# Performance work log

Measured on AMD Instinct MI355X. Metric: run time of the kernel, lower is better.

Reference implementation:

```python
import jax, jax.numpy as jnp
import numpy as np

D_MODEL = 1024
NUM_HEADS = 16
HEAD_DIM = 64
INNER = NUM_HEADS * HEAD_DIM


def setup_inputs() -> dict:
    key = jax.random.key(0)
    k_x, k_q, k_k, k_v, k_o = jax.random.split(key, 5)
    B, T = 4, 2048
    s = 1.0 / np.sqrt(D_MODEL)
    return {
        "x": jax.random.normal(k_x, (B, T, D_MODEL), dtype=jnp.float32),
        "W_q": jax.random.uniform(k_q, (D_MODEL, INNER), dtype=jnp.float32, minval=-s, maxval=s),
        "W_k": jax.random.uniform(k_k, (D_MODEL, INNER), dtype=jnp.float32, minval=-s, maxval=s),
        "W_v": jax.random.uniform(k_v, (D_MODEL, INNER), dtype=jnp.float32, minval=-s, maxval=s),
        "W_o": jax.random.uniform(k_o, (INNER, D_MODEL), dtype=jnp.float32, minval=-s, maxval=s),
    }


def reference(x, W_q, W_k, W_v, W_o):
    B, T, _ = x.shape
    scale = HEAD_DIM ** -0.5
    # project and split heads: [B, H, T, Dh]
    q = (x @ W_q).reshape(B, T, NUM_HEADS, HEAD_DIM).transpose(0, 2, 1, 3)
    k = (x @ W_k).reshape(B, T, NUM_HEADS, HEAD_DIM).transpose(0, 2, 1, 3)
    v = (x @ W_v).reshape(B, T, NUM_HEADS, HEAD_DIM).transpose(0, 2, 1, 3)
    scores = jnp.einsum("bhqd,bhkd->bhqk", q, k) * scale  # [B,H,T,T]
    causal = jnp.tril(jnp.ones((T, T), dtype=bool))
    scores = jnp.where(causal, scores, -jnp.inf)
    probs = jax.nn.softmax(scores, axis=-1)
    ctx = jnp.einsum("bhqk,bhkd->bhqd", probs, v)
    ctx = ctx.transpose(0, 2, 1, 3).reshape(B, T, INNER)
    return ctx @ W_o
```

## Files before the change

kernel.cpp:

```cpp
#include <hip/hip_runtime.h>


typedef short  short8  __attribute__((ext_vector_type(8)));
typedef short  short4v __attribute__((ext_vector_type(4)));
typedef float  floatx4 __attribute__((ext_vector_type(4)));
typedef unsigned uint2v __attribute__((ext_vector_type(2)));
typedef unsigned uintx4 __attribute__((ext_vector_type(4)));

#define T_SZ 2048
#define DM   1024

#define QSCALE 0.18033688011112042f

__device__ __forceinline__ short f2bf(float f) {
  unsigned u = __float_as_uint(f);
  u += 0x7fffu + ((u >> 16) & 1u);
  return (short)(u >> 16);
}

#if defined(__has_builtin) && __has_builtin(__builtin_amdgcn_cvt_pk_bf16_f32)
typedef __bf16 bf16x2_t __attribute__((ext_vector_type(2)));
__device__ __forceinline__ unsigned pack_bf(float lo, float hi) {
  return __builtin_bit_cast(unsigned, __builtin_amdgcn_cvt_pk_bf16_f32(lo, hi));
}
#else
__device__ __forceinline__ unsigned pack_bf(float lo, float hi) {
  return __builtin_amdgcn_perm(__float_as_uint(hi) + 0x8000u,
                               __float_as_uint(lo) + 0x8000u, 0x07060302u);
}
#endif

#if defined(__has_builtin) && __has_builtin(__builtin_amdgcn_exp2f)
__device__ __forceinline__ float fexp2(float x) { return __builtin_amdgcn_exp2f(x); }
#else
__device__ __forceinline__ float fexp2(float x) { return exp2f(x); }
#endif

#if defined(__has_builtin)
#if __has_builtin(__builtin_amdgcn_permlane32_swap) && __has_builtin(__builtin_amdgcn_permlane16_swap)
#define HAVE_PLSWAP 1
#endif
#endif

#ifdef HAVE_PLSWAP
__device__ __forceinline__ short8 pswap_build(unsigned w0, unsigned w1,
                                              unsigned w2, unsigned w3) {
  auto r02 = __builtin_amdgcn_permlane32_swap(w0, w2, false, false);
  auto r13 = __builtin_amdgcn_permlane32_swap(w1, w3, false, false);
  auto d02 = __builtin_amdgcn_permlane16_swap(r02[0], r02[1], false, false);
  auto d13 = __builtin_amdgcn_permlane16_swap(r13[0], r13[1], false, false);
  uintx4 pd;
  pd.x = d02[0]; pd.y = d13[0]; pd.z = d02[1]; pd.w = d13[1];
  return __builtin_bit_cast(short8, pd);
}
#endif

__device__ __forceinline__ void gll16(const void* g, void* l) {
  __builtin_amdgcn_global_load_lds((const __attribute__((address_space(1))) void*)g,
                                   (__attribute__((address_space(3))) void*)l, 16, 0, 0);
}

#define SBAR() asm volatile("s_barrier" ::: "memory")
#define WLG()  asm volatile("s_waitcnt lgkmcnt(0)" ::: "memory")
#define WV6()  asm volatile("s_waitcnt vmcnt(6)" ::: "memory")
#define WV0()  asm volatile("s_waitcnt vmcnt(0)" ::: "memory")

__global__ void cvt_kernel(const float* __restrict__ s0, const float* __restrict__ s1,
                           const float* __restrict__ s2, const float* __restrict__ s3,
                           short* __restrict__ dst,
                           const float* __restrict__ x, short* __restrict__ xb) {
  const int tx = threadIdx.x, ty = threadIdx.y;
  if (blockIdx.z == 4) {
    const int tid = ty * 32 + tx;
    const int blk = blockIdx.y * 32 + blockIdx.x;
    int i = (blk * 256 + tid) * 4;
#pragma unroll
    for (int j = 0; j < 8; ++j) {
      const float4 v = *(const float4*)(x + i);
      short4v o;
      o.x = f2bf(v.x); o.y = f2bf(v.y); o.z = f2bf(v.z); o.w = f2bf(v.w);
      *(short4v*)(xb + i) = o;
      i += 1048576;
    }
    return;
  }
  const float* srcs[4] = {s0, s1, s2, s3};
  const float* src = srcs[blockIdx.z];
  short* d = dst + (size_t)blockIdx.z * 1048576;
  __shared__ float tile[32][33];
  const int n_base = blockIdx.x * 32, k_base = blockIdx.y * 32;
#pragma unroll
  for (int j = 0; j < 4; ++j)
    tile[ty + j * 8][tx] = src[(size_t)(k_base + ty + j * 8) * 1024 + n_base + tx];
  __syncthreads();
#pragma unroll
  for (int j = 0; j < 4; ++j)
    d[(size_t)(n_base + ty + j * 8) * 1024 + k_base + tx] = f2bf(tile[tx][ty + j * 8]);
}

__global__ __launch_bounds__(512, 2) void gemm_qkvT(
    const short* __restrict__ Wt, const short* __restrict__ xb,
    short* __restrict__ obf, short* __restrict__ vt) {
  __shared__ short As[2 * 128 * 64];
  __shared__ short Bs[2 * 256 * 64];
  const int tid  = threadIdx.x;
  const int w    = tid >> 6, lane = tid & 63;
  const int quad = lane >> 4, l15 = lane & 15;
  const int wr   = w >> 2, wc = w & 3;
  const int fx   = l15 & 7;
  const int lid  = (int)blockIdx.x;
  const int xcd  = lid & 7, idx = lid >> 3;
  const int m0   = (idx >> 2) * 128;
  const int n0   = (xcd * 4 + (idx & 3)) * 256;
  const int srow = tid >> 3;
  const int scol = ((tid & 7) ^ (srow & 7)) * 8;

  const short* Ag = Wt + (size_t)(m0 + srow) * 1024 + scol;
  const short* Bg = xb + (size_t)(n0 + srow) * 1024 + scol;

  floatx4 acc[4][4] = {};
  short8 af[2][2], bf[4][2];

#define STG_A(slot, kb) do { \
    short* _lb = &As[(slot) * 8192 + tid * 8]; \
    gll16(Ag + (kb), _lb); \
    gll16(Ag + (size_t)(64 * 1024) + (kb), _lb + 4096); \
  } while (0)
#define STG_B(slot, h, kb) do { \
    short* _lb = &Bs[(slot) * 16384 + (h) * 8192 + tid * 8]; \
    const short* _gp = Bg + (size_t)(h) * (128 * 1024) + (kb); \
    gll16(_gp, _lb); \
    gll16(_gp + (size_t)(64 * 1024), _lb + 4096); \
  } while (0)
#define LDA2(slot, ih) do { \
    _Pragma("unroll") for (int ii = 0; ii < 2; ++ii) \
    _Pragma("unroll") for (int s = 0; s < 2; ++s) \
      af[ii][s] = *(const short8*)&As[(slot) * 8192 + \
          (wr * 64 + (ih) * 32 + ii * 16 + l15) * 64 + ((s * 4 + quad) ^ fx) * 8]; \
  } while (0)
#define LDB8(slot) do { \
    _Pragma("unroll") for (int j = 0; j < 4; ++j) \
    _Pragma("unroll") for (int s = 0; s < 2; ++s) \
      bf[j][s] = *(const short8*)&Bs[(slot) * 16384 + \
          (wc * 64 + j * 16 + l15) * 64 + ((s * 4 + quad) ^ fx) * 8]; \
  } while (0)
#define MMQ(ih, jh) do { \
    __builtin_amdgcn_s_setprio(1); \
    _Pragma("unroll") for (int ii = 0; ii < 2; ++ii) \
    _Pragma("unroll") for (int jj = 0; jj < 2; ++jj) \
    _Pragma("unroll") for (int s = 0; s < 2; ++s) \
      acc[(ih) * 2 + ii][(jh) * 2 + jj] = __builtin_amdgcn_mfma_f32_16x16x32_bf16( \
          af[ii][s], bf[(jh) * 2 + jj][s], acc[(ih) * 2 + ii][(jh) * 2 + jj], 0, 0, 0); \
    __builtin_amdgcn_s_setprio(0); \
  } while (0)

  STG_B(0, 0, 0);  STG_B(0, 1, 0);  STG_A(0, 0);
  STG_B(1, 0, 64); STG_B(1, 1, 64); STG_A(1, 64);
  WV6(); SBAR();

  for (int t = 0; t < 8; ++t) {
    const int kn2 = (2 * t + 2) * 64;
    const int kn3 = (2 * t + 3) * 64;
    const bool mre = (t < 7);
    LDA2(0, 0); LDB8(0);
    SBAR(); WLG(); MMQ(0, 0); SBAR();
    if (mre) STG_B(0, 0, kn2);
    SBAR(); MMQ(0, 1); SBAR();
    LDA2(0, 1);
    if (mre) STG_B(0, 1, kn2);
    SBAR(); WLG(); MMQ(1, 0); SBAR();
    if (mre) { STG_A(0, kn2); WV6(); } else { WV0(); }
    SBAR(); MMQ(1, 1); SBAR();
    LDA2(1, 0); LDB8(1);
    SBAR(); WLG(); MMQ(0, 0); SBAR();
    if (mre) STG_B(1, 0, kn3);
    SBAR(); MMQ(0, 1); SBAR();
    LDA2(1, 1);
    if (mre) STG_B(1, 1, kn3);
    SBAR(); WLG(); MMQ(1, 0); SBAR();
    if (mre) { STG_A(1, kn3); WV6(); }
    SBAR(); MMQ(1, 1); SBAR();
  }

  const int wsel = m0 >> 10;
  const int nn0  = (m0 & 1023) + wr * 64;
  if (wsel < 2) {
    const float scale = (wsel == 0) ? QSCALE : 1.0f;
    short* outw = obf + (size_t)wsel * (64u * 2048u * 64u);
#pragma unroll
    for (int i = 0; i < 4; ++i) {
      const int nn = nn0 + i * 16 + quad * 4;
      const int h = nn >> 6, d = nn & 63;
#pragma unroll
      for (int j = 0; j < 4; ++j) {
        const int tg = n0 + wc * 64 + j * 16 + l15;
        const int b = tg >> 11, tt = tg & 2047;
        short4v o4;
#pragma unroll
        for (int r = 0; r < 4; ++r) o4[r] = f2bf(acc[i][j][r] * scale);
        *(short4v*)(outw + (((size_t)(b * 16 + h) * 2048 + tt) << 6) + d) = o4;
      }
    }
  } else {
#pragma unroll
    for (int i = 0; i < 4; ++i) {
      const int nn = nn0 + i * 16 + quad * 4;
      const int h = nn >> 6, d = nn & 63;
#pragma unroll
      for (int j = 0; j < 4; ++j) {
        const int tg = n0 + wc * 64 + j * 16 + l15;
        const int b = tg >> 11, tt = tg & 2047;
#pragma unroll
        for (int r = 0; r < 4; ++r)
          vt[(((size_t)(b * 16 + h) * 64 + d + r) << 11) + tt] = f2bf(acc[i][j][r]);
      }
    }
  }
#undef STG_A
#undef STG_B
#undef LDA2
#undef LDB8
#undef MMQ
}

__global__ __launch_bounds__(512, 2) void gemm8W(
    const short* __restrict__ A, const short* __restrict__ B,
    float* __restrict__ of) {
  __shared__ short As[2 * 128 * 64];
  __shared__ short Bs[2 * 256 * 64];
  const int tid  = threadIdx.x;
  const int w    = tid >> 6, lane = tid & 63;
  const int quad = lane >> 4, l15 = lane & 15;
  const int wr   = w >> 2, wc = w & 3;
  const int fx   = l15 & 7;
  const int lid  = (int)blockIdx.x;
  const int xcd  = lid & 7, idx = lid >> 3;
  const int m0   = (idx >> 2) * 128;
  const int n0   = (xcd * 4 + (idx & 3)) * 256;
  const int srow = tid >> 3;
  const int scol = ((tid & 7) ^ (srow & 7)) * 8;

  const short* Ag = A + (size_t)(m0 + srow) * 1024 + scol;
  const short* Bg = B + (size_t)(n0 + srow) * 1024 + scol;

  floatx4 acc[4][4] = {};
  short8 af[4][2], bf[4][2];

#define STG_A(slot, kb) do { \
    short* _lb = &As[(slot) * 8192 + tid * 8]; \
    const short* _gp = Ag + (kb); \
    gll16(_gp, _lb); \
    gll16(_gp + (size_t)(64 * 1024), _lb + 4096); \
  } while (0)
#define STG_B(slot, kb) do { \
    short* _lb = &Bs[(slot) * 16384 + tid * 8]; \
    const short* _gp = Bg + (kb); \
    gll16(_gp,                         _lb); \
    gll16(_gp + (size_t)( 64 * 1024), _lb + 4096); \
    gll16(_gp + (size_t)(128 * 1024), _lb + 8192); \
    gll16(_gp + (size_t)(192 * 1024), _lb + 12288); \
  } while (0)
#define LDA_ALL(slot) do { \
    _Pragma("unroll") for (int ii = 0; ii < 4; ++ii) \
    _Pragma("unroll") for (int s = 0; s < 2; ++s) \
      af[ii][s] = *(const short8*)&As[(slot) * 8192 + \
          (wr * 64 + ii * 16 + l15) * 64 + ((s * 4 + quad) ^ fx) * 8]; \
  } while (0)
#define LDB_ALL(slot) do { \
    _Pragma("unroll") for (int j = 0; j < 4; ++j) \
    _Pragma("unroll") for (int s = 0; s < 2; ++s) \
      bf[j][s] = *(const short8*)&Bs[(slot) * 16384 + \
          (wc * 64 + j * 16 + l15) * 64 + ((s * 4 + quad) ^ fx) * 8]; \
  } while (0)
#define MMH(ih) do { \
    __builtin_amdgcn_s_setprio(1); \
    _Pragma("unroll") for (int i2 = 0; i2 < 2; ++i2) \
    _Pragma("unroll") for (int j = 0; j < 4; ++j) \
    _Pragma("unroll") for (int s = 0; s < 2; ++s) \
      acc[(ih) * 2 + i2][j] = __builtin_amdgcn_mfma_f32_16x16x32_bf16( \
          af[(ih) * 2 + i2][s], bf[j][s], acc[(ih) * 2 + i2][j], 0, 0, 0); \
    __builtin_amdgcn_s_setprio(0); \
  } while (0)

  STG_B(0, 0);  STG_A(0, 0);
  STG_B(1, 64); STG_A(1, 64);
  WV6(); SBAR();

  for (int t = 0; t < 8; ++t) {
    const int kn2 = (2 * t + 2) * 64;
    const int kn3 = (2 * t + 3) * 64;
    const bool mre = (t < 7);
    LDA_ALL(0); LDB_ALL(0);
    SBAR(); WLG();
    MMH(0);
    SBAR();
    if (mre) STG_B(0, kn2);
    if (mre) STG_A(0, kn2);
    MMH(1);
    if (mre) WV6(); else WV0();
    SBAR();
    LDA_ALL(1); LDB_ALL(1);
    SBAR(); WLG();
    MMH(0);
    SBAR();
    if (mre) STG_B(1, kn3);
    if (mre) STG_A(1, kn3);
    MMH(1);
    if (mre) WV6();
    SBAR();
  }

  const int nn0 = m0 + wr * 64;
#pragma unroll
  for (int i = 0; i < 4; ++i) {
    const int nn = nn0 + i * 16 + quad * 4;
#pragma unroll
    for (int j = 0; j < 4; ++j) {
      const int tg = n0 + wc * 64 + j * 16 + l15;
      float4 o4;
      o4.x = acc[i][j][0]; o4.y = acc[i][j][1];
      o4.z = acc[i][j][2]; o4.w = acc[i][j][3];
      *(float4*)(of + (size_t)tg * 1024 + nn) = o4;
    }
  }
#undef STG_A
#undef STG_B
#undef LDA_ALL
#undef LDB_ALL
#undef MMH
}

__global__ __launch_bounds__(512, 4) void attn_kernel(
    const short* __restrict__ Qg, const short* __restrict__ Kg,
    const short* __restrict__ Vt, short* __restrict__ ctx) {
  __shared__ short Ks[128 * 72];
  __shared__ short Vs[80 * 136];
#ifndef HAVE_PLSWAP
  __shared__ short Ps[8 * 32 * 40];
#endif

  const int tid  = threadIdx.x;
  const int w    = tid >> 6, lane = tid & 63;
  const int quad = lane >> 4, l15 = lane & 15;
  const int bh = (int)blockIdx.x + 8 * ((int)blockIdx.y & 7);
  const int g  = (int)blockIdx.y >> 3;
  const int qb = (g < 4) ? (7 - g) : (g - 4);
  const int b  = bh >> 4, h = bh & 15;

  const size_t base = (size_t)bh * (T_SZ * 64);
  const short* Qb  = Qg + base;
  const short* Kb  = Kg + base;
  const short* Vtb = Vt + base;
#ifndef HAVE_PLSWAP
  short* Pw = &Ps[w * 1280];
#endif

  const int skr = tid >> 2, skp = (tid & 3) * 16;
  const int svr = tid >> 3, svp = (tid & 7) * 16;

  if (tid < 256) {
    const int rr = 64 + (tid >> 4), cb = (tid & 15) * 8;
    const short vv = (tid < 16) ? (short)0x3F80 : (short)0;
    short8 fill;
#pragma unroll
    for (int j = 0; j < 8; ++j) fill[j] = vv;
    *(short8*)&Vs[rr * 136 + cb] = fill;
  }

  const int rowA = qb * 256 + w * 32;
  const int rowB = rowA + 16;
  const int ktmax = 2 * qb + 2;

  const short8 qA0 = *(const short8*)(Qb + (size_t)(rowA + l15) * 64 + quad * 8);
  const short8 qA1 = *(const short8*)(Qb + (size_t)(rowA + l15) * 64 + 32 + quad * 8);
  const short8 qB0 = *(const short8*)(Qb + (size_t)(rowB + l15) * 64 + quad * 8);
  const short8 qB1 = *(const short8*)(Qb + (size_t)(rowB + l15) * 64 + 32 + quad * 8);

  floatx4 OA[4] = {}, OB[4] = {};
  floatx4 O5A = {}, O5B = {};

  short8 kR[2], vR[2];
  kR[0] = *(const short8*)(Kb + (size_t)skr * 64 + skp);
  kR[1] = *(const short8*)(Kb + (size_t)skr * 64 + skp + 8);
  vR[0] = *(const short8*)(Vtb + (size_t)svr * 2048 + svp);
  vR[1] = *(const short8*)(Vtb + (size_t)svr * 2048 + svp + 8);

  for (int kt = 0; kt < ktmax; ++kt) {
    const int k0 = kt << 7;
    __syncthreads();
    *(short8*)&Ks[skr * 72 + skp]     = kR[0];
    *(short8*)&Ks[skr * 72 + skp + 8] = kR[1];
    *(short8*)&Vs[svr * 136 + svp]     = vR[0];
    *(short8*)&Vs[svr * 136 + svp + 8] = vR[1];
    if (kt + 1 < ktmax) {
      const int kn = (kt + 1) << 7;
      kR[0] = *(const short8*)(Kb + (size_t)(kn + skr) * 64 + skp);
      kR[1] = *(const short8*)(Kb + (size_t)(kn + skr) * 64 + skp + 8);
      vR[0] = *(const short8*)(Vtb + (size_t)svr * 2048 + kn + svp);
      vR[1] = *(const short8*)(Vtb + (size_t)svr * 2048 + kn + svp + 8);
    }
    __syncthreads();

    const int dkA = rowA - k0;
    if (dkA < 0) continue;
    const int dkB = dkA + 16;
    const int limA = dkA + l15, limB = limA + 16;
    const int naA = min(8, (dkA >> 4) + 1), nchA = (naA + 1) >> 1;
    const int naB = min(8, (dkB >> 4) + 1), nchB = (naB + 1) >> 1;

#ifdef HAVE_PLSWAP
#pragma unroll
    for (int c = 0; c < 4; ++c) {
      if (c < nchB) {
        unsigned wB0, wB1, wB2 = 0, wB3 = 0;
        unsigned wA0 = 0, wA1 = 0, wA2 = 0, wA3 = 0;
        {
          const int mt = 2 * c;
          const short8 kf0 = *(const short8*)&Ks[(mt * 16 + l15) * 72 + quad * 8];
          const short8 kf1 = *(const short8*)&Ks[(mt * 16 + l15) * 72 + 32 + quad * 8];
          {
            floatx4 s = {};
            s = __builtin_amdgcn_mfma_f32_16x16x32_bf16(kf0, qB0, s, 0, 0, 0);
            s = __builtin_amdgcn_mfma_f32_16x16x32_bf16(kf1, qB1, s, 0, 0, 0);
            if (mt * 16 + 15 > dkB) {
#pragma unroll
              for (int r = 0; r < 4; ++r)
                if (mt * 16 + quad * 4 + r > limB) s[r] = -1e30f;
            }
            wB0 = pack_bf(fexp2(s[0]), fexp2(s[1]));
            wB1 = pack_bf(fexp2(s[2]), fexp2(s[3]));
          }
          if (c < nchA) {
            floatx4 s = {};
            s = __builtin_amdgcn_mfma_f32_16x16x32_bf16(kf0, qA0, s, 0, 0, 0);
            s = __builtin_amdgcn_mfma_f32_16x16x32_bf16(kf1, qA1, s, 0, 0, 0);
            if (mt * 16 + 15 > dkA) {
#pragma unroll
              for (int r = 0; r < 4; ++r)
                if (mt * 16 + quad * 4 + r > limA) s[r] = -1e30f;
            }
            wA0 = pack_bf(fexp2(s[0]), fexp2(s[1]));
            wA1 = pack_bf(fexp2(s[2]), fexp2(s[3]));
          }
        }
        if (2 * c + 1 < naB) {
          const int mt = 2 * c + 1;
          const short8 kf0 = *(const short8*)&Ks[(mt * 16 + l15) * 72 + quad * 8];
          const short8 kf1 = *(const short8*)&Ks[(mt * 16 + l15) * 72 + 32 + quad * 8];
          {
            floatx4 s = {};
            s = __builtin_amdgcn_mfma_f32_16x16x32_bf16(kf0, qB0, s, 0, 0, 0);
            s = __builtin_amdgcn_mfma_f32_16x16x32_bf16(kf1, qB1, s, 0, 0, 0);
            if (mt * 16 + 15 > dkB) {
#pragma unroll
              for (int r = 0; r < 4; ++r)
                if (mt * 16 + quad * 4 + r > limB) s[r] = -1e30f;
            }
            wB2 = pack_bf(fexp2(s[0]), fexp2(s[1]));
            wB3 = pack_bf(fexp2(s[2]), fexp2(s[3]));
          }
          if (c < nchA && mt < naA) {
            floatx4 s = {};
            s = __builtin_amdgcn_mfma_f32_16x16x32_bf16(kf0, qA0, s, 0, 0, 0);
            s = __builtin_amdgcn_mfma_f32_16x16x32_bf16(kf1, qA1, s, 0, 0, 0);
            if (mt * 16 + 15 > dkA) {
#pragma unroll
              for (int r = 0; r < 4; ++r)
                if (mt * 16 + quad * 4 + r > limA) s[r] = -1e30f;
            }
            wA2 = pack_bf(fexp2(s[0]), fexp2(s[1]));
            wA3 = pack_bf(fexp2(s[2]), fexp2(s[3]));
          }
        }
        const short8 pfB = pswap_build(wB0, wB1, wB2, wB3);
        const int vcol = c * 32 + quad * 8;
        const short8 vfl = *(const short8*)&Vs[(64 + l15) * 136 + vcol];
        short8 vf[4];
#pragma unroll
        for (int dt = 0; dt < 4; ++dt)
          vf[dt] = *(const short8*)&Vs[(dt * 16 + l15) * 136 + vcol];
#pragma unroll
        for (int dt = 0; dt < 4; ++dt)
          OB[dt] = __builtin_amdgcn_mfma_f32_16x16x32_bf16(vf[dt], pfB, OB[dt], 0, 0, 0);
        O5B = __builtin_amdgcn_mfma_f32_16x16x32_bf16(vfl, pfB, O5B, 0, 0, 0);
        if (c < nchA) {
          const short8 pfA = pswap_build(wA0, wA1, wA2, wA3);
#pragma unroll
          for (int dt = 0; dt < 4; ++dt)
            OA[dt] = __builtin_amdgcn_mfma_f32_16x16x32_bf16(vf[dt], pfA, OA[dt], 0, 0, 0);
          O5A = __builtin_amdgcn_mfma_f32_16x16x32_bf16(vfl, pfA, O5A, 0, 0, 0);
        }
      }
    }
#else
#pragma unroll
    for (int c = 0; c < 4; ++c) {
      if (c < nchB) {
#pragma unroll
        for (int mm = 0; mm < 2; ++mm) {
          const int mt = 2 * c + mm;
          const int pa = l15 * 40 + mm * 16 + quad * 4;
          const int pb = (16 + l15) * 40 + mm * 16 + quad * 4;
          const bool aB = (mt * 16 < dkB + 16);
          const bool aA = (mt * 16 < dkA + 16);
          if (aB) {
            const short8 kf0 = *(const short8*)&Ks[(mt * 16 + l15) * 72 + quad * 8];
            const short8 kf1 = *(const short8*)&Ks[(mt * 16 + l15) * 72 + 32 + quad * 8];
            {
              floatx4 s = {};
              s = __builtin_amdgcn_mfma_f32_16x16x32_bf16(kf0, qB0, s, 0, 0, 0);
              s = __builtin_amdgcn_mfma_f32_16x16x32_bf16(kf1, qB1, s, 0, 0, 0);
              if (mt * 16 + 15 > dkB) {
#pragma unroll
                for (int r = 0; r < 4; ++r)
                  if (mt * 16 + quad * 4 + r > limB) s[r] = -1e30f;
              }
              floatx4 e;
#pragma unroll
              for (int r = 0; r < 4; ++r) e[r] = fexp2(s[r]);
              uint2v pd;
              pd.x = pack_bf(e[0], e[1]);
              pd.y = pack_bf(e[2], e[3]);
              *(uint2v*)&Pw[pb] = pd;
            }
            if (c < nchA) {
              if (aA) {
                floatx4 s = {};
                s = __builtin_amdgcn_mfma_f32_16x16x32_bf16(kf0, qA0, s, 0, 0, 0);
                s = __builtin_amdgcn_mfma_f32_16x16x32_bf16(kf1, qA1, s, 0, 0, 0);
                if (mt * 16 + 15 > dkA) {
#pragma unroll
                  for (int r = 0; r < 4; ++r)
                    if (mt * 16 + quad * 4 + r > limA) s[r] = -1e30f;
                }
                floatx4 e;
#pragma unroll
                for (int r = 0; r < 4; ++r) e[r] = fexp2(s[r]);
                uint2v pd;
                pd.x = pack_bf(e[0], e[1]);
                pd.y = pack_bf(e[2], e[3]);
                *(uint2v*)&Pw[pa] = pd;
              } else {
                uint2v z; z.x = 0; z.y = 0;
                *(uint2v*)&Pw[pa] = z;
              }
            }
          } else {
            uint2v z; z.x = 0; z.y = 0;
            *(uint2v*)&Pw[pb] = z;
            if (c < nchA) *(uint2v*)&Pw[pa] = z;
          }
        }
        const int vcol = c * 32 + quad * 8;
        const short8 vfl = *(const short8*)&Vs[(64 + l15) * 136 + vcol];
        short8 vf[4];
#pragma unroll
        for (int dt = 0; dt < 4; ++dt)
          vf[dt] = *(const short8*)&Vs[(dt * 16 + l15) * 136 + vcol];
        const short8 pfB = *(const short8*)&Pw[(16 + l15) * 40 + quad * 8];
#pragma unroll
        for (int dt = 0; dt < 4; ++dt)
          OB[dt] = __builtin_amdgcn_mfma_f32_16x16x32_bf16(vf[dt], pfB, OB[dt], 0, 0, 0);
        O5B = __builtin_amdgcn_mfma_f32_16x16x32_bf16(vfl, pfB, O5B, 0, 0, 0);
        if (c < nchA) {
          const short8 pfA = *(const short8*)&Pw[l15 * 40 + quad * 8];
#pragma unroll
          for (int dt = 0; dt < 4; ++dt)
            OA[dt] = __builtin_amdgcn_mfma_f32_16x16x32_bf16(vf[dt], pfA, OA[dt], 0, 0, 0);
          O5A = __builtin_amdgcn_mfma_f32_16x16x32_bf16(vfl, pfA, O5A, 0, 0, 0);
        }
      }
    }
#endif
  }

  {
    const float lA = __shfl(O5A[0], l15);
    const float invA = 1.0f / lA;
    const int t = rowA + l15;
    short* cb = ctx + (((size_t)(b * T_SZ + t)) << 10) + h * 64 + quad * 4;
#pragma unroll
    for (int dt = 0; dt < 4; ++dt) {
      short4v o4;
#pragma unroll
      for (int r = 0; r < 4; ++r) o4[r] = f2bf(OA[dt][r] * invA);
      *(short4v*)(cb + dt * 16) = o4;
    }
  }
  {
    const float lB = __shfl(O5B[0], l15);
    const float invB = 1.0f / lB;
    const int t = rowB + l15;
    short* cb = ctx + (((size_t)(b * T_SZ + t)) << 10) + h * 64 + quad * 4;
#pragma unroll
    for (int dt = 0; dt < 4; ++dt) {
      short4v o4;
#pragma unroll
      for (int r = 0; r < 4; ++r) o4[r] = f2bf(OB[dt][r] * invB);
      *(short4v*)(cb + dt * 16) = o4;
    }
  }
}

extern "C" void kernel_launch(void* const* d_in, const int* in_sizes, int n_in,
                              void* d_out, int out_size, void* d_ws, size_t ws_size,
                              hipStream_t stream) {
  const float* x  = (const float*)d_in[0];
  const float* Wq = (const float*)d_in[1];
  const float* Wk = (const float*)d_in[2];
  const float* Wv = (const float*)d_in[3];
  const float* Wo = (const float*)d_in[4];
  float* out = (float*)d_out;

  short* ws  = (short*)d_ws;
  short* xb  = ws;
  short* Wt  = ws + 8388608;
  short* Qb  = Wt + 4 * 1048576;
  short* Kb  = Qb + 8388608;
  short* Vt  = Kb + 8388608;
  short* ctx = xb;

  cvt_kernel<<<dim3(32, 32, 5), dim3(32, 8), 0, stream>>>(Wq, Wk, Wv, Wo, Wt, x, xb);
  gemm_qkvT<<<dim3(768), 512, 0, stream>>>(Wt, xb, Qb, Vt);
  attn_kernel<<<dim3(8, 64), 512, 0, stream>>>(Qb, Kb, Vt, ctx);
  gemm8W<<<dim3(256), 512, 0, stream>>>(Wt + 3 * 1048576, ctx, out);
}
```

Measured before the change: 237.7 us.

## Split long causal query blocks across two KV halves and combine with atomics

Attention blocks for the four longest causal query tiles now each process only half of their KV range. The halves accumulate unnormalized outputs and row sums with fp32 atomics into scratch space borrowed from the output and ctx buffers. A new zero kernel clears that scratch beforehand, and a new combine kernel normalizes and converts the result to bf16 afterwards. This evens out per-block work and raises the grid to 768 blocks, and the attention launch-bounds occupancy hint goes from 4 to 6. In exchange it adds two extra launches, atomic traffic, and a risk of register spills under the tighter occupancy target.

```diff
diff --git a/kernel.cpp b/kernel.cpp
--- a/kernel.cpp
+++ b/kernel.cpp
@@ -96,6 +96,36 @@
 #pragma unroll
   for (int j = 0; j < 4; ++j)
     d[(size_t)(n_base + ty + j * 8) * 1024 + k_base + tx] = f2bf(tile[tx][ty + j * 8]);
+}
+
+__global__ void zero_kernel(float* __restrict__ outp, short* __restrict__ ctx) {
+  const int g = (int)blockIdx.x * 256 + (int)threadIdx.x;
+  const int off = g * 4;
+  float4 z; z.x = 0.f; z.y = 0.f; z.z = 0.f; z.w = 0.f;
+#pragma unroll
+  for (int bb = 0; bb < 4; ++bb)
+    *(float4*)(outp + (((size_t)(bb * 2048 + 1024)) << 10) + off) = z;
+  if (g < 65536) {
+    const int bb = g >> 14, t = 1024 + ((g >> 4) & 1023), hh = g & 15;
+    ((float*)(ctx + (((size_t)(bb * 2048 + t)) << 10)))[hh] = 0.f;
+  }
+}
+
+__global__ void combine_kernel(const float* __restrict__ outp, short* __restrict__ ctx) {
+  __shared__ float ls[16];
+  const int bid = (int)blockIdx.x;
+  const int bb = bid >> 10, t = 1024 + (bid & 1023);
+  const size_t row = ((size_t)(bb * 2048 + t)) << 10;
+  const float* lrow = (const float*)(ctx + row);
+  if (threadIdx.x < 16) ls[threadIdx.x] = lrow[threadIdx.x];
+  __syncthreads();
+  const int c0 = (int)threadIdx.x * 4;
+  const float4 o = *(const float4*)(outp + row + c0);
+  const float inv = 1.0f / ls[c0 >> 6];
+  short4v o4;
+  o4[0] = f2bf(o.x * inv); o4[1] = f2bf(o.y * inv);
+  o4[2] = f2bf(o.z * inv); o4[3] = f2bf(o.w * inv);
+  *(short4v*)(ctx + row + c0) = o4;
 }
 
 __global__ __launch_bounds__(512, 2) void gemm_qkvT(
@@ -330,9 +360,10 @@
 #undef MMH
 }
 
-__global__ __launch_bounds__(512, 4) void attn_kernel(
+__global__ __launch_bounds__(512, 6) void attn_kernel(
     const short* __restrict__ Qg, const short* __restrict__ Kg,
-    const short* __restrict__ Vt, short* __restrict__ ctx) {
+    const short* __restrict__ Vt, short* __restrict__ ctx,
+    float* __restrict__ outp) {
   __shared__ short Ks[128 * 72];
   __shared__ short Vs[80 * 136];
 #ifndef HAVE_PLSWAP
@@ -343,8 +374,12 @@
   const int w    = tid >> 6, lane = tid & 63;
   const int quad = lane >> 4, l15 = lane & 15;
   const int bh = (int)blockIdx.x + 8 * ((int)blockIdx.y & 7);
-  const int g  = (int)blockIdx.y >> 3;
-  const int qb = (g < 4) ? (7 - g) : (g - 4);
+  const int u  = (int)blockIdx.y >> 3;
+  int qb, kt0, kte, isSplit;
+  if (u < 8) { qb = 7 - (u >> 1); const int mid = qb + 1;
+               kt0 = (u & 1) ? mid : 0; kte = (u & 1) ? (2 * qb + 2) : mid;
+               isSplit = 1; }
+  else       { qb = 11 - u; kt0 = 0; kte = 2 * qb + 2; isSplit = 0; }
   const int b  = bh >> 4, h = bh & 15;
 
   const size_t base = (size_t)bh * (T_SZ * 64);
@@ -369,7 +404,6 @@
 
   const int rowA = qb * 256 + w * 32;
   const int rowB = rowA + 16;
-  const int ktmax = 2 * qb + 2;
 
   const short8 qA0 = *(const short8*)(Qb + (size_t)(rowA + l15) * 64 + quad * 8);
   const short8 qA1 = *(const short8*)(Qb + (size_t)(rowA + l15) * 64 + 32 + quad * 8);
@@ -380,19 +414,22 @@
   floatx4 O5A = {}, O5B = {};
 
   short8 kR[2], vR[2];
-  kR[0] = *(const short8*)(Kb + (size_t)skr * 64 + skp);
-  kR[1] = *(const short8*)(Kb + (size_t)skr * 64 + skp + 8);
-  vR[0] = *(const short8*)(Vtb + (size_t)svr * 2048 + svp);
-  vR[1] = *(const short8*)(Vtb + (size_t)svr * 2048 + svp + 8);
-
-  for (int kt = 0; kt < ktmax; ++kt) {
+  {
+    const int kc = kt0 << 7;
+    kR[0] = *(const short8*)(Kb + (size_t)(kc + skr) * 64 + skp);
+    kR[1] = *(const short8*)(Kb + (size_t)(kc + skr) * 64 + skp + 8);
+    vR[0] = *(const short8*)(Vtb + (size_t)svr * 2048 + kc + svp);
+    vR[1] = *(const short8*)(Vtb + (size_t)svr * 2048 + kc + svp + 8);
+  }
+
+  for (int kt = kt0; kt < kte; ++kt) {
     const int k0 = kt << 7;
     __syncthreads();
     *(short8*)&Ks[skr * 72 + skp]     = kR[0];
     *(short8*)&Ks[skr * 72 + skp + 8] = kR[1];
     *(short8*)&Vs[svr * 136 + svp]     = vR[0];
     *(short8*)&Vs[svr * 136 + svp + 8] = vR[1];
-    if (kt + 1 < ktmax) {
+    if (kt + 1 < kte) {
       const int kn = (kt + 1) << 7;
       kR[0] = *(const short8*)(Kb + (size_t)(kn + skr) * 64 + skp);
       kR[1] = *(const short8*)(Kb + (size_t)(kn + skr) * 64 + skp + 8);
@@ -574,30 +611,57 @@
 #endif
   }
 
-  {
-    const float lA = __shfl(O5A[0], l15);
-    const float invA = 1.0f / lA;
-    const int t = rowA + l15;
-    short* cb = ctx + (((size_t)(b * T_SZ + t)) << 10) + h * 64 + quad * 4;
-#pragma unroll
-    for (int dt = 0; dt < 4; ++dt) {
-      short4v o4;
-#pragma unroll
-      for (int r = 0; r < 4; ++r) o4[r] = f2bf(OA[dt][r] * invA);
-      *(short4v*)(cb + dt * 16) = o4;
-    }
-  }
-  {
-    const float lB = __shfl(O5B[0], l15);
-    const float invB = 1.0f / lB;
-    const int t = rowB + l15;
-    short* cb = ctx + (((size_t)(b * T_SZ + t)) << 10) + h * 64 + quad * 4;
-#pragma unroll
-    for (int dt = 0; dt < 4; ++dt) {
-      short4v o4;
-#pragma unroll
-      for (int r = 0; r < 4; ++r) o4[r] = f2bf(OB[dt][r] * invB);
-      *(short4v*)(cb + dt * 16) = o4;
+  if (isSplit) {
+    {
+      const float lA = __shfl(O5A[0], l15);
+      const int t = rowA + l15;
+      float* ob = outp + (((size_t)(b * T_SZ + t)) << 10) + h * 64 + quad * 4;
+#pragma unroll
+      for (int dt = 0; dt < 4; ++dt)
+#pragma unroll
+        for (int r = 0; r < 4; ++r)
+          atomicAdd(ob + dt * 16 + r, OA[dt][r]);
+      if (quad == 0)
+        atomicAdd((float*)(ctx + (((size_t)(b * T_SZ + t)) << 10)) + h, lA);
+    }
+    {
+      const float lB = __shfl(O5B[0], l15);
+      const int t = rowB + l15;
+      float* ob = outp + (((size_t)(b * T_SZ + t)) << 10) + h * 64 + quad * 4;
+#pragma unroll
+      for (int dt = 0; dt < 4; ++dt)
+#pragma unroll
+        for (int r = 0; r < 4; ++r)
+          atomicAdd(ob + dt * 16 + r, OB[dt][r]);
+      if (quad == 0)
+        atomicAdd((float*)(ctx + (((size_t)(b * T_SZ + t)) << 10)) + h, lB);
+    }
+  } else {
+    {
+      const float lA = __shfl(O5A[0], l15);
+      const float invA = 1.0f / lA;
+      const int t = rowA + l15;
+      short* cb = ctx + (((size_t)(b * T_SZ + t)) << 10) + h * 64 + quad * 4;
+#pragma unroll
+      for (int dt = 0; dt < 4; ++dt) {
+        short4v o4;
+#pragma unroll
+        for (int r = 0; r < 4; ++r) o4[r] = f2bf(OA[dt][r] * invA);
+        *(short4v*)(cb + dt * 16) = o4;
+      }
+    }
+    {
+      const float lB = __shfl(O5B[0], l15);
+      const float invB = 1.0f / lB;
+      const int t = rowB + l15;
+      short* cb = ctx + (((size_t)(b * T_SZ + t)) << 10) + h * 64 + quad * 4;
+#pragma unroll
+      for (int dt = 0; dt < 4; ++dt) {
+        short4v o4;
+#pragma unroll
+        for (int r = 0; r < 4; ++r) o4[r] = f2bf(OB[dt][r] * invB);
+        *(short4v*)(cb + dt * 16) = o4;
+      }
     }
   }
 }
@@ -622,6 +686,8 @@
 
   cvt_kernel<<<dim3(32, 32, 5), dim3(32, 8), 0, stream>>>(Wq, Wk, Wv, Wo, Wt, x, xb);
   gemm_qkvT<<<dim3(768), 512, 0, stream>>>(Wt, xb, Qb, Vt);
-  attn_kernel<<<dim3(8, 64), 512, 0, stream>>>(Qb, Kb, Vt, ctx);
+  zero_kernel<<<dim3(1024), 256, 0, stream>>>(out, ctx);
+  attn_kernel<<<dim3(8, 96), 512, 0, stream>>>(Qb, Kb, Vt, ctx, out);
+  combine_kernel<<<dim3(4096), 256, 0, stream>>>(out, ctx);
   gemm8W<<<dim3(256), 512, 0, stream>>>(Wt + 3 * 1048576, ctx, out);
 }
```

Result: slower. 450.6 us (+89.5%).
